# Optimization experiments

Measured on AMD Instinct MI355X. Metric: run time of the kernel, lower is better.

## Reference

```python
import jax, jax.numpy as jnp
import numpy as np


def _skew_relative(QE):
    # QE: [B, H, N, 2N-1] -> [B, H, N, N] relative-position skew (Music-Transformer style)
    B, H, N, L = QE.shape  # L == 2N - 1
    x = jnp.pad(QE, ((0, 0), (0, 0), (0, 0), (0, 1))).reshape(B, H, N * (L + 1))
    x = jnp.pad(x, ((0, 0), (0, 0), (0, N - 1))).reshape(B, H, N + 1, 2 * N - 1)
    return x[:, :, :N, -N:]


def setup_inputs() -> dict:
    key = jax.random.key(0)
    ks = jax.random.split(key, 8)
    B, N, D, H, dh = 8, 1024, 512, 8, 64
    W_SCALE = 0.02
    return {
        "x": jax.random.normal(ks[0], (B, N, D), jnp.float32),
        "phase": jax.random.uniform(ks[1], (B, H, N, 1), jnp.float32),
        "E_rel": jax.random.normal(ks[2], (2 * N - 1, dh), jnp.float32) * 0.05,
        "W_q": jax.random.normal(ks[3], (H * dh, D), jnp.float32) * W_SCALE,
        "W_k": jax.random.normal(ks[4], (H * dh, D), jnp.float32) * W_SCALE,
        "W_v": jax.random.normal(ks[5], (H * dh, D), jnp.float32) * W_SCALE,
        "W_o": jax.random.normal(ks[6], (D, H * dh), jnp.float32) * W_SCALE,
        "b_o": jnp.zeros((D,), jnp.float32),
    }


def reference(x, phase, E_rel, W_q, W_k, W_v, W_o, b_o):
    B, N, _ = x.shape
    H = phase.shape[1]
    dh = W_q.shape[0] // H
    scale = 1.0 / (dh ** 0.5)

    def heads(W):  # [B,N,H*dh] -> [B,H,N,dh]
        return (x @ W.T).reshape(B, N, H, dh).transpose(0, 2, 1, 3)

    Q, K, V = heads(W_q), heads(W_k), heads(W_v)
    attn = jnp.einsum('bhnd,bhmd->bhnm', Q, K)
    attn = attn + _skew_relative(jnp.einsum('bhnd,ld->bhnl', Q, E_rel))
    attn = jax.nn.softmax(attn * scale, axis=-1)
    out = jnp.einsum('bhnm,bhmd->bhnd', attn, V) * phase  # phase-modulated AV
    out = out.transpose(0, 2, 1, 3).reshape(B, N, H * dh)
    return out @ W_o.T + b_o  # dropout is identity in eval mode
```

## Files before the change

### kernel.cpp

```cpp
#include <hip/hip_runtime.h>


typedef __bf16 bf16x8 __attribute__((ext_vector_type(8)));
typedef __bf16 bf16x4 __attribute__((ext_vector_type(4)));
typedef float  f32x4  __attribute__((ext_vector_type(4)));
typedef float  f32x16 __attribute__((ext_vector_type(16)));

#if __has_builtin(__builtin_amdgcn_exp2f)
#define EXP2(x) __builtin_amdgcn_exp2f(x)
#else
#define EXP2(x) exp2f(x)
#endif

#define QSCALE 0.18033688011f

#define GLOAD_LDS16(g, l)                                                      \
    __builtin_amdgcn_global_load_lds(                                          \
        (const __attribute__((address_space(1))) unsigned int*)(g),            \
        (__attribute__((address_space(3))) unsigned int*)(l), 16, 0, 0)


__global__ __launch_bounds__(256) void cvt_all(const float* __restrict__ x,
                                               const float* __restrict__ E,
                                               const float* __restrict__ wq,
                                               const float* __restrict__ wk,
                                               const float* __restrict__ wv,
                                               const float* __restrict__ wo,
                                               __bf16* __restrict__ xb,
                                               __bf16* __restrict__ Ef,
                                               __bf16* __restrict__ wqkv,
                                               __bf16* __restrict__ wob) {
    int i = blockIdx.x * 256 + threadIdx.x;
    if (i >= 1081328 ? i < 1343472 : i < 1048576) {
        const float* s; __bf16* d; int off;
        if      (i < 1048576) { s = x;  d = xb;            off = i; }
        else if (i < 1146864) { s = wq; d = wqkv;          off = i - 1081328; }
        else if (i < 1212400) { s = wk; d = wqkv + 262144; off = i - 1146864; }
        else if (i < 1277936) { s = wv; d = wqkv + 524288; off = i - 1212400; }
        else                  { s = wo; d = wob;           off = i - 1277936; }
        float4 v = *(const float4*)(s + (size_t)off * 4);
        bf16x4 o;
        o[0] = (__bf16)v.x; o[1] = (__bf16)v.y; o[2] = (__bf16)v.z; o[3] = (__bf16)v.w;
        *(bf16x4*)(d + (size_t)off * 4) = o;
    } else if (i >= 1048576 && i < 1081328) {
        int off = i - 1048576;
        float4 v = *(const float4*)(E + (size_t)off * 4);
        int e0i = off * 4;
        int l = e0i >> 6, d0 = e0i & 63;
        int t32 = l >> 5, cq = l & 31, ks = d0 >> 4, hf = (d0 >> 3) & 1, j = d0 & 7;
        bf16x4 o;
        o[0] = (__bf16)v.x; o[1] = (__bf16)v.y; o[2] = (__bf16)v.z; o[3] = (__bf16)v.w;
        *(bf16x4*)(Ef + ((size_t)((t32 * 4 + ks) * 64) + hf * 32 + cq) * 8 + j) = o;
    }
}

__global__ __launch_bounds__(256) void gemm_qkv(const __bf16* __restrict__ X,
                                                const __bf16* __restrict__ W,
                                                __bf16* __restrict__ Qb,
                                                __bf16* __restrict__ Kf,
                                                __bf16* __restrict__ Vf) {
    __shared__ __bf16 Xs[128][64];
    __shared__ __bf16 Ws[128][64];
    const int tid = threadIdx.x;
    const int wave = tid >> 6, lane = tid & 63;
    const int col = lane & 15, quad = lane >> 4;
    const int m_base = blockIdx.x * 128;
    const int j_base = blockIdx.y * 128;
    const bool qk = (j_base < 1024);
    const int wm = (wave & 1) * 64;
    const int wn = (wave >> 1) * 64;
    const f32x4 fz = {0.f, 0.f, 0.f, 0.f};
    f32x4 acc[4][4];
#pragma unroll
    for (int i = 0; i < 4; ++i)
#pragma unroll
        for (int j = 0; j < 4; ++j) acc[i][j] = fz;

    for (int k0 = 0; k0 < 512; k0 += 64) {
#pragma unroll
        for (int p = 0; p < 4; ++p) {
            int s = tid + p * 256;
            int row = s >> 3, cc = (s & 7) * 8;
            GLOAD_LDS16(X + (size_t)(m_base + row) * 512 + k0 + cc, &Xs[0][0] + (size_t)s * 8);
            GLOAD_LDS16(W + (size_t)(j_base + row) * 512 + k0 + cc, &Ws[0][0] + (size_t)s * 8);
        }
        __syncthreads();
#pragma unroll
        for (int kk = 0; kk < 64; kk += 32) {
            bf16x8 xa[4], wb[4];
#pragma unroll
            for (int i = 0; i < 4; ++i) xa[i] = *(const bf16x8*)(&Xs[wm + i * 16 + col][kk + quad * 8]);
#pragma unroll
            for (int j = 0; j < 4; ++j) wb[j] = *(const bf16x8*)(&Ws[wn + j * 16 + col][kk + quad * 8]);
            if (qk) {
#pragma unroll
                for (int i = 0; i < 4; ++i)
#pragma unroll
                    for (int j = 0; j < 4; ++j)
                        acc[i][j] = __builtin_amdgcn_mfma_f32_16x16x32_bf16(wb[i], xa[j], acc[i][j], 0, 0, 0);
            } else {
#pragma unroll
                for (int i = 0; i < 4; ++i)
#pragma unroll
                    for (int j = 0; j < 4; ++j)
                        acc[i][j] = __builtin_amdgcn_mfma_f32_16x16x32_bf16(xa[i], wb[j], acc[i][j], 0, 0, 0);
            }
        }
        __syncthreads();
    }
    if (qk) {
#pragma unroll
        for (int i = 0; i < 4; ++i) {
#pragma unroll
            for (int j = 0; j < 4; ++j) {
                int jabs = j_base + wn + i * 16 + quad * 4;
                int m = m_base + wm + j * 16 + col;
                int b_ = m >> 10, n = m & 1023;
                int rem = jabs & 511, h = rem >> 6, d = rem & 63;
                bf16x4 v;
                if (jabs < 512) {
                    v[0] = (__bf16)(acc[i][j][0] * QSCALE);
                    v[1] = (__bf16)(acc[i][j][1] * QSCALE);
                    v[2] = (__bf16)(acc[i][j][2] * QSCALE);
                    v[3] = (__bf16)(acc[i][j][3] * QSCALE);
                    *(bf16x4*)(Qb + (((size_t)b_ * 8 + h) * 1024 + n) * 64 + d) = v;
                } else {
                    v[0] = (__bf16)acc[i][j][0]; v[1] = (__bf16)acc[i][j][1];
                    v[2] = (__bf16)acc[i][j][2]; v[3] = (__bf16)acc[i][j][3];
                    int t32 = n >> 5, cq = n & 31, ks = d >> 4, hf = (d >> 3) & 1, jj = d & 7;
                    *(bf16x4*)(Kf + (size_t)(b_ * 8 + h) * 65536 +
                               ((size_t)((t32 * 4 + ks) * 64) + hf * 32 + cq) * 8 + jj) = v;
                }
            }
        }
    } else {
#pragma unroll
        for (int i = 0; i < 4; ++i) {
#pragma unroll
            for (int j = 0; j < 4; ++j) {
                int m = m_base + wm + i * 16 + quad * 4;
                int b_ = m >> 10, n = m & 1023;
                int jabs = j_base + wn + j * 16 + col;
                int rem = jabs & 511, h = rem >> 6, d = rem & 63;
                int t64 = n >> 6, ks = (n >> 4) & 3, hf = (n >> 3) & 1, jj = n & 7;
                int dhalf = d >> 5, cq = d & 31;
                bf16x4 v;
                v[0] = (__bf16)acc[i][j][0]; v[1] = (__bf16)acc[i][j][1];
                v[2] = (__bf16)acc[i][j][2]; v[3] = (__bf16)acc[i][j][3];
                *(bf16x4*)(Vf + (size_t)(b_ * 8 + h) * 65536 +
                           ((size_t)(((t64 * 4 + ks) * 2 + dhalf) * 64) + hf * 32 + cq) * 8 + jj) = v;
            }
        }
    }
}

#define FLASH_HALF(T, KC0, KC1, KN0, KN1)                                              \
  {                                                                                    \
    const int t_ = (T);                                                                \
    const int teB_ = te0 + 2 * t_ + 1;                                                 \
    bf16x8 e1f[4], e2f[4], v0f[4], v1f[4];                                             \
    _Pragma("unroll")                                                                  \
    for (int ks = 0; ks < 4; ++ks) {                                                   \
      e1f[ks] = *(const bf16x8*)(Ef + ((size_t)((teB_ * 4 + ks) * 64) + lane) * 8);    \
      e2f[ks] = *(const bf16x8*)(Ef + ((size_t)(((teB_ + 1) * 4 + ks) * 64) + lane) * 8); \
    }                                                                                  \
    _Pragma("unroll")                                                                  \
    for (int ks = 0; ks < 4; ++ks) {                                                   \
      v0f[ks] = *(const bf16x8*)(Vfb + ((size_t)(((t_ * 4 + ks) * 2 + 0) * 64) + lane) * 8); \
      v1f[ks] = *(const bf16x8*)(Vfb + ((size_t)(((t_ * 4 + ks) * 2 + 1) * 64) + lane) * 8); \
    }                                                                                  \
    f32x16 qeB = z16, qeC = z16, s0 = z16, s1 = z16;                                   \
    _Pragma("unroll")                                                                  \
    for (int ks = 0; ks < 4; ++ks) {                                                   \
      s0 = __builtin_amdgcn_mfma_f32_32x32x16_bf16(a_q[ks], KC0[ks], s0, 0, 0, 0);     \
      s1 = __builtin_amdgcn_mfma_f32_32x32x16_bf16(a_q[ks], KC1[ks], s1, 0, 0, 0);     \
    }                                                                                  \
    const int t32n_ = (((T) + 1) & 15) * 2;                                            \
    _Pragma("unroll")                                                                  \
    for (int ks = 0; ks < 4; ++ks) {                                                   \
      KN0[ks] = *(const bf16x8*)(Kfb + ((size_t)((t32n_ * 4 + ks) * 64) + lane) * 8);  \
      KN1[ks] = *(const bf16x8*)(Kfb + ((size_t)(((t32n_ + 1) * 4 + ks) * 64) + lane) * 8); \
    }                                                                                  \
    _Pragma("unroll")                                                                  \
    for (int ks = 0; ks < 4; ++ks) {                                                   \
      qeB = __builtin_amdgcn_mfma_f32_32x32x16_bf16(a_q[ks], e1f[ks], qeB, 0, 0, 0);   \
      qeC = __builtin_amdgcn_mfma_f32_32x32x16_bf16(a_q[ks], e2f[ks], qeC, 0, 0, 0);   \
    }                                                                                  \
    _Pragma("unroll")                                                                  \
    for (int r = 0; r < 16; ++r) {                                                     \
      int row = (r & 3) + 8 * (r >> 2) + 4 * half;                                     \
      int tt = colq + 31 - row;                                                        \
      int src = (tt & 31) | (half << 5);                                               \
      float shB = __shfl(qeB[r], src, 64);                                             \
      float shC = __shfl(qeC[r], src, 64);                                             \
      bool sel = (tt >= 32);                                                           \
      float rel0 = sel ? shB : shA[r];                                                 \
      float rel1 = sel ? shC : shB;                                                    \
      float p0 = EXP2(s0[r] + rel0);                                                   \
      float p1 = EXP2(s1[r] + rel1);                                                   \
      rowsum[r] += p0 + p1;                                                            \
      Pw[w][row][colq]      = (__bf16)p0;                                              \
      Pw[w][row][32 + colq] = (__bf16)p1;                                              \
      shA[r] = shC;                                                                    \
    }                                                                                  \
    asm volatile("s_waitcnt lgkmcnt(0)" ::: "memory");                                 \
    _Pragma("unroll")                                                                  \
    for (int ks = 0; ks < 4; ++ks) {                                                   \
      bf16x8 pa = *(const bf16x8*)(&Pw[w][colq][ks * 16 + half * 8]);                  \
      o0 = __builtin_amdgcn_mfma_f32_32x32x16_bf16(pa, v0f[ks], o0, 0, 0, 0);          \
      o1 = __builtin_amdgcn_mfma_f32_32x32x16_bf16(pa, v1f[ks], o1, 0, 0, 0);          \
    }                                                                                  \
    asm volatile("" ::: "memory");                                                     \
  }

__global__ __launch_bounds__(128, 2) void flash_kernel(const __bf16* __restrict__ Qb,
                                                       const __bf16* __restrict__ Kf,
                                                       const __bf16* __restrict__ Vf,
                                                       const __bf16* __restrict__ Ef,
                                                       const float* __restrict__ phase,
                                                       __bf16* __restrict__ Ob) {
    const int bh = blockIdx.y;
    const int n0 = blockIdx.x * 64;
    const int w = threadIdx.x >> 6, lane = threadIdx.x & 63;
    const int colq = lane & 31, half = lane >> 5;
    const int nbase = n0 + w * 32;

    __shared__ __bf16 Pw[2][32][72];

    f32x16 z16;
#pragma unroll
    for (int i = 0; i < 16; ++i) z16[i] = 0.f;

    bf16x8 a_q[4];
#pragma unroll
    for (int ks = 0; ks < 4; ++ks)
        a_q[ks] = *(const bf16x8*)(Qb + ((size_t)bh * 1024 + nbase + colq) * 64 + ks * 16 + half * 8);

    f32x16 o0 = z16, o1 = z16;
    float rowsum[16];
#pragma unroll
    for (int i = 0; i < 16; ++i) rowsum[i] = 0.f;

    const __bf16* Kfb = Kf + (size_t)bh * 65536;
    const __bf16* Vfb = Vf + (size_t)bh * 65536;

    const int te0 = (992 - nbase) >> 5;

    bf16x8 kA0[4], kA1[4], kB0[4], kB1[4];
#pragma unroll
    for (int ks = 0; ks < 4; ++ks) {
        kA0[ks] = *(const bf16x8*)(Kfb + ((size_t)((0 * 4 + ks) * 64) + lane) * 8);
        kA1[ks] = *(const bf16x8*)(Kfb + ((size_t)((1 * 4 + ks) * 64) + lane) * 8);
    }

    float shA[16];
    {
        f32x16 qeA = z16;
#pragma unroll
        for (int ks = 0; ks < 4; ++ks) {
            bf16x8 e = *(const bf16x8*)(Ef + ((size_t)((te0 * 4 + ks) * 64) + lane) * 8);
            qeA = __builtin_amdgcn_mfma_f32_32x32x16_bf16(a_q[ks], e, qeA, 0, 0, 0);
        }
#pragma unroll
        for (int r = 0; r < 16; ++r) {
            int row = (r & 3) + 8 * (r >> 2) + 4 * half;
            int tt = colq + 31 - row;
            int src = (tt & 31) | (half << 5);
            shA[r] = __shfl(qeA[r], src, 64);
        }
    }

#pragma unroll 1
    for (int tt2 = 0; tt2 < 8; ++tt2) {
        FLASH_HALF(2 * tt2,     kA0, kA1, kB0, kB1)
        FLASH_HALF(2 * tt2 + 1, kB0, kB1, kA0, kA1)
    }

    const int b_ = bh >> 3, hh = bh & 7;
#pragma unroll
    for (int r = 0; r < 16; ++r) {
        float l = rowsum[r];
        l += __shfl_xor(l, 1, 32);
        l += __shfl_xor(l, 2, 32);
        l += __shfl_xor(l, 4, 32);
        l += __shfl_xor(l, 8, 32);
        l += __shfl_xor(l, 16, 32);
        int row = (r & 3) + 8 * (r >> 2) + 4 * half;
        float f = phase[(size_t)bh * 1024 + nbase + row] / l;
        Pw[w][row][colq]      = (__bf16)(o0[r] * f);
        Pw[w][row][32 + colq] = (__bf16)(o1[r] * f);
    }
    asm volatile("s_waitcnt lgkmcnt(0)" ::: "memory");
    {
        int row = lane >> 1, dseg = lane & 1;
        bf16x8 u0 = *(const bf16x8*)(&Pw[w][row][dseg * 32]);
        bf16x8 u1 = *(const bf16x8*)(&Pw[w][row][dseg * 32 + 8]);
        bf16x8 u2 = *(const bf16x8*)(&Pw[w][row][dseg * 32 + 16]);
        bf16x8 u3 = *(const bf16x8*)(&Pw[w][row][dseg * 32 + 24]);
        size_t obase = ((size_t)b_ * 1024 + nbase + row) * 512 + hh * 64 + dseg * 32;
        *(bf16x8*)(Ob + obase)      = u0;
        *(bf16x8*)(Ob + obase + 8)  = u1;
        *(bf16x8*)(Ob + obase + 16) = u2;
        *(bf16x8*)(Ob + obase + 24) = u3;
    }
}

__global__ __launch_bounds__(256) void gemm_out(const __bf16* __restrict__ X,
                                                const __bf16* __restrict__ W,
                                                const float* __restrict__ bo,
                                                float* __restrict__ out) {
    __shared__ __bf16 Xs[128][64];
    __shared__ __bf16 Ws[64][64];
    const int tid = threadIdx.x;
    const int wave = tid >> 6, lane = tid & 63;
    const int col = lane & 15, quad = lane >> 4;
    const int m_base = blockIdx.x * 128;
    const int j_base = blockIdx.y * 64;
    const int wm = (wave & 1) * 64;
    const int wn = (wave >> 1) * 32;
    const f32x4 fz = {0.f, 0.f, 0.f, 0.f};
    f32x4 acc[2][4];
#pragma unroll
    for (int i = 0; i < 2; ++i)
#pragma unroll
        for (int j = 0; j < 4; ++j) acc[i][j] = fz;

    for (int k0 = 0; k0 < 512; k0 += 64) {
#pragma unroll
        for (int p = 0; p < 4; ++p) {
            int s = tid + p * 256;
            int row = s >> 3, cc = (s & 7) * 8;
            GLOAD_LDS16(X + (size_t)(m_base + row) * 512 + k0 + cc, &Xs[0][0] + (size_t)s * 8);
        }
#pragma unroll
        for (int p = 0; p < 2; ++p) {
            int s = tid + p * 256;
            int row = s >> 3, cc = (s & 7) * 8;
            GLOAD_LDS16(W + (size_t)(j_base + row) * 512 + k0 + cc, &Ws[0][0] + (size_t)s * 8);
        }
        __syncthreads();
#pragma unroll
        for (int kk = 0; kk < 64; kk += 32) {
            bf16x8 xa[4], wb[2];
#pragma unroll
            for (int j = 0; j < 4; ++j) xa[j] = *(const bf16x8*)(&Xs[wm + j * 16 + col][kk + quad * 8]);
#pragma unroll
            for (int i = 0; i < 2; ++i) wb[i] = *(const bf16x8*)(&Ws[wn + i * 16 + col][kk + quad * 8]);
#pragma unroll
            for (int i = 0; i < 2; ++i)
#pragma unroll
                for (int j = 0; j < 4; ++j)
                    acc[i][j] = __builtin_amdgcn_mfma_f32_16x16x32_bf16(wb[i], xa[j], acc[i][j], 0, 0, 0);
        }
        __syncthreads();
    }
#pragma unroll
    for (int i = 0; i < 2; ++i) {
#pragma unroll
        for (int j = 0; j < 4; ++j) {
            int jabs = j_base + wn + i * 16 + quad * 4;
            int m = m_base + wm + j * 16 + col;
            f32x4 bv = *(const f32x4*)(bo + jabs);
            f32x4 o = acc[i][j] + bv;
            *(f32x4*)(out + (size_t)m * 512 + jabs) = o;
        }
    }
}

extern "C" void kernel_launch(void* const* d_in, const int* in_sizes, int n_in,
                              void* d_out, int out_size, void* d_ws, size_t ws_size,
                              hipStream_t stream) {
    (void)in_sizes; (void)n_in; (void)out_size; (void)ws_size;
    const float* x     = (const float*)d_in[0];
    const float* phase = (const float*)d_in[1];
    const float* E_rel = (const float*)d_in[2];
    const float* W_q   = (const float*)d_in[3];
    const float* W_k   = (const float*)d_in[4];
    const float* W_v   = (const float*)d_in[5];
    const float* W_o   = (const float*)d_in[6];
    const float* b_o   = (const float*)d_in[7];
    float* out = (float*)d_out;

    char* ws = (char*)d_ws;
    __bf16* xb   = (__bf16*)(ws);
    __bf16* wqkv = (__bf16*)(ws + 8388608);
    __bf16* wob  = (__bf16*)(ws + 9961472);
    __bf16* Ef   = (__bf16*)(ws + 10485760);
    __bf16* Qb   = (__bf16*)(ws + 10747904);
    __bf16* Kf   = (__bf16*)(ws + 19136512);
    __bf16* Vf   = (__bf16*)(ws + 27525120);
    __bf16* Ob   = (__bf16*)(ws + 35913728);

    cvt_all<<<dim3(5249), dim3(256), 0, stream>>>(x, E_rel, W_q, W_k, W_v, W_o,
                                                  xb, Ef, wqkv, wob);
    gemm_qkv<<<dim3(64, 12), dim3(256), 0, stream>>>(xb, wqkv, Qb, Kf, Vf);
    flash_kernel<<<dim3(16, 64), dim3(128), 0, stream>>>(Qb, Kf, Vf, Ef, phase, Ob);
    gemm_out<<<dim3(64, 8), dim3(256), 0, stream>>>(Ob, wob, b_o, out);
}
```

Baseline: 170.8 us.

## Double-buffer LDS tiles in QKV and output projection GEMMs

Both projection GEMMs now hold two LDS buffers and issue the global-to-LDS loads for the next K tile before computing on the current one. Explicit vmcnt waits and raw s_barrier calls replace the __syncthreads pairs, so the load latency overlaps with MFMA work. This doubles LDS use per block, which may lower occupancy, and the hand-counted vmcnt values must match the number of outstanding loads.

```diff
diff --git a/kernel.cpp b/kernel.cpp
--- a/kernel.cpp
+++ b/kernel.cpp
@@ -54,13 +54,49 @@
     }
 }
 
+#define QKV_STAGE(BUF, K0)                                                     \
+    _Pragma("unroll")                                                          \
+    for (int p = 0; p < 4; ++p) {                                              \
+        int s = tid + p * 256;                                                 \
+        int row = s >> 3, cc = (s & 7) * 8;                                    \
+        GLOAD_LDS16(X + (size_t)(m_base + row) * 512 + (K0) + cc,              \
+                    &Xs[BUF][0][0] + (size_t)s * 8);                           \
+        GLOAD_LDS16(W + (size_t)(j_base + row) * 512 + (K0) + cc,              \
+                    &Ws[BUF][0][0] + (size_t)s * 8);                           \
+    }
+
+#define QKV_COMPUTE(BUF)                                                       \
+    _Pragma("unroll")                                                          \
+    for (int kk = 0; kk < 64; kk += 32) {                                      \
+        bf16x8 xa[4], wb[4];                                                   \
+        _Pragma("unroll")                                                      \
+        for (int i = 0; i < 4; ++i)                                            \
+            xa[i] = *(const bf16x8*)(&Xs[BUF][wm + i * 16 + col][kk + quad * 8]); \
+        _Pragma("unroll")                                                      \
+        for (int j = 0; j < 4; ++j)                                            \
+            wb[j] = *(const bf16x8*)(&Ws[BUF][wn + j * 16 + col][kk + quad * 8]); \
+        if (qk) {                                                              \
+            _Pragma("unroll")                                                  \
+            for (int i = 0; i < 4; ++i)                                        \
+                _Pragma("unroll")                                              \
+                for (int j = 0; j < 4; ++j)                                    \
+                    acc[i][j] = __builtin_amdgcn_mfma_f32_16x16x32_bf16(wb[i], xa[j], acc[i][j], 0, 0, 0); \
+        } else {                                                               \
+            _Pragma("unroll")                                                  \
+            for (int i = 0; i < 4; ++i)                                        \
+                _Pragma("unroll")                                              \
+                for (int j = 0; j < 4; ++j)                                    \
+                    acc[i][j] = __builtin_amdgcn_mfma_f32_16x16x32_bf16(xa[i], wb[j], acc[i][j], 0, 0, 0); \
+        }                                                                      \
+    }
+
 __global__ __launch_bounds__(256) void gemm_qkv(const __bf16* __restrict__ X,
                                                 const __bf16* __restrict__ W,
                                                 __bf16* __restrict__ Qb,
                                                 __bf16* __restrict__ Kf,
                                                 __bf16* __restrict__ Vf) {
-    __shared__ __bf16 Xs[128][64];
-    __shared__ __bf16 Ws[128][64];
+    __shared__ __bf16 Xs[2][128][64];
+    __shared__ __bf16 Ws[2][128][64];
     const int tid = threadIdx.x;
     const int wave = tid >> 6, lane = tid & 63;
     const int col = lane & 15, quad = lane >> 4;
@@ -76,38 +112,20 @@
 #pragma unroll
         for (int j = 0; j < 4; ++j) acc[i][j] = fz;
 
-    for (int k0 = 0; k0 < 512; k0 += 64) {
-#pragma unroll
-        for (int p = 0; p < 4; ++p) {
-            int s = tid + p * 256;
-            int row = s >> 3, cc = (s & 7) * 8;
-            GLOAD_LDS16(X + (size_t)(m_base + row) * 512 + k0 + cc, &Xs[0][0] + (size_t)s * 8);
-            GLOAD_LDS16(W + (size_t)(j_base + row) * 512 + k0 + cc, &Ws[0][0] + (size_t)s * 8);
-        }
-        __syncthreads();
-#pragma unroll
-        for (int kk = 0; kk < 64; kk += 32) {
-            bf16x8 xa[4], wb[4];
-#pragma unroll
-            for (int i = 0; i < 4; ++i) xa[i] = *(const bf16x8*)(&Xs[wm + i * 16 + col][kk + quad * 8]);
-#pragma unroll
-            for (int j = 0; j < 4; ++j) wb[j] = *(const bf16x8*)(&Ws[wn + j * 16 + col][kk + quad * 8]);
-            if (qk) {
-#pragma unroll
-                for (int i = 0; i < 4; ++i)
-#pragma unroll
-                    for (int j = 0; j < 4; ++j)
-                        acc[i][j] = __builtin_amdgcn_mfma_f32_16x16x32_bf16(wb[i], xa[j], acc[i][j], 0, 0, 0);
-            } else {
-#pragma unroll
-                for (int i = 0; i < 4; ++i)
-#pragma unroll
-                    for (int j = 0; j < 4; ++j)
-                        acc[i][j] = __builtin_amdgcn_mfma_f32_16x16x32_bf16(xa[i], wb[j], acc[i][j], 0, 0, 0);
-            }
-        }
-        __syncthreads();
-    }
+    QKV_STAGE(0, 0)
+#pragma unroll 1
+    for (int it = 0; it < 7; ++it) {
+        const int cur = it & 1;
+        if (cur == 0) { QKV_STAGE(1, (it + 1) * 64) } else { QKV_STAGE(0, (it + 1) * 64) }
+        asm volatile("s_waitcnt vmcnt(16)" ::: "memory");
+        __builtin_amdgcn_s_barrier();
+        if (cur == 0) { QKV_COMPUTE(0) } else { QKV_COMPUTE(1) }
+        __builtin_amdgcn_s_barrier();
+    }
+    asm volatile("s_waitcnt vmcnt(0)" ::: "memory");
+    __builtin_amdgcn_s_barrier();
+    QKV_COMPUTE(1)
+
     if (qk) {
 #pragma unroll
         for (int i = 0; i < 4; ++i) {
@@ -305,12 +323,45 @@
     }
 }
 
+#define OUT_STAGE(BUF, K0)                                                     \
+    _Pragma("unroll")                                                          \
+    for (int p = 0; p < 4; ++p) {                                              \
+        int s = tid + p * 256;                                                 \
+        int row = s >> 3, cc = (s & 7) * 8;                                    \
+        GLOAD_LDS16(X + (size_t)(m_base + row) * 512 + (K0) + cc,              \
+                    &Xs[BUF][0][0] + (size_t)s * 8);                           \
+    }                                                                          \
+    _Pragma("unroll")                                                          \
+    for (int p = 0; p < 2; ++p) {                                              \
+        int s = tid + p * 256;                                                 \
+        int row = s >> 3, cc = (s & 7) * 8;                                    \
+        GLOAD_LDS16(W + (size_t)(j_base + row) * 512 + (K0) + cc,              \
+                    &Ws[BUF][0][0] + (size_t)s * 8);                           \
+    }
+
+#define OUT_COMPUTE(BUF)                                                       \
+    _Pragma("unroll")                                                          \
+    for (int kk = 0; kk < 64; kk += 32) {                                      \
+        bf16x8 xa[4], wb[2];                                                   \
+        _Pragma("unroll")                                                      \
+        for (int j = 0; j < 4; ++j)                                            \
+            xa[j] = *(const bf16x8*)(&Xs[BUF][wm + j * 16 + col][kk + quad * 8]); \
+        _Pragma("unroll")                                                      \
+        for (int i = 0; i < 2; ++i)                                            \
+            wb[i] = *(const bf16x8*)(&Ws[BUF][wn + i * 16 + col][kk + quad * 8]); \
+        _Pragma("unroll")                                                      \
+        for (int i = 0; i < 2; ++i)                                            \
+            _Pragma("unroll")                                                  \
+            for (int j = 0; j < 4; ++j)                                        \
+                acc[i][j] = __builtin_amdgcn_mfma_f32_16x16x32_bf16(wb[i], xa[j], acc[i][j], 0, 0, 0); \
+    }
+
 __global__ __launch_bounds__(256) void gemm_out(const __bf16* __restrict__ X,
                                                 const __bf16* __restrict__ W,
                                                 const float* __restrict__ bo,
                                                 float* __restrict__ out) {
-    __shared__ __bf16 Xs[128][64];
-    __shared__ __bf16 Ws[64][64];
+    __shared__ __bf16 Xs[2][128][64];
+    __shared__ __bf16 Ws[2][64][64];
     const int tid = threadIdx.x;
     const int wave = tid >> 6, lane = tid & 63;
     const int col = lane & 15, quad = lane >> 4;
@@ -325,35 +376,20 @@
 #pragma unroll
         for (int j = 0; j < 4; ++j) acc[i][j] = fz;
 
-    for (int k0 = 0; k0 < 512; k0 += 64) {
-#pragma unroll
-        for (int p = 0; p < 4; ++p) {
-            int s = tid + p * 256;
-            int row = s >> 3, cc = (s & 7) * 8;
-            GLOAD_LDS16(X + (size_t)(m_base + row) * 512 + k0 + cc, &Xs[0][0] + (size_t)s * 8);
-        }
-#pragma unroll
-        for (int p = 0; p < 2; ++p) {
-            int s = tid + p * 256;
-            int row = s >> 3, cc = (s & 7) * 8;
-            GLOAD_LDS16(W + (size_t)(j_base + row) * 512 + k0 + cc, &Ws[0][0] + (size_t)s * 8);
-        }
-        __syncthreads();
-#pragma unroll
-        for (int kk = 0; kk < 64; kk += 32) {
-            bf16x8 xa[4], wb[2];
-#pragma unroll
-            for (int j = 0; j < 4; ++j) xa[j] = *(const bf16x8*)(&Xs[wm + j * 16 + col][kk + quad * 8]);
-#pragma unroll
-            for (int i = 0; i < 2; ++i) wb[i] = *(const bf16x8*)(&Ws[wn + i * 16 + col][kk + quad * 8]);
-#pragma unroll
-            for (int i = 0; i < 2; ++i)
-#pragma unroll
-                for (int j = 0; j < 4; ++j)
-                    acc[i][j] = __builtin_amdgcn_mfma_f32_16x16x32_bf16(wb[i], xa[j], acc[i][j], 0, 0, 0);
-        }
-        __syncthreads();
-    }
+    OUT_STAGE(0, 0)
+#pragma unroll 1
+    for (int it = 0; it < 7; ++it) {
+        const int cur = it & 1;
+        if (cur == 0) { OUT_STAGE(1, (it + 1) * 64) } else { OUT_STAGE(0, (it + 1) * 64) }
+        asm volatile("s_waitcnt vmcnt(6)" ::: "memory");
+        __builtin_amdgcn_s_barrier();
+        if (cur == 0) { OUT_COMPUTE(0) } else { OUT_COMPUTE(1) }
+        __builtin_amdgcn_s_barrier();
+    }
+    asm volatile("s_waitcnt vmcnt(0)" ::: "memory");
+    __builtin_amdgcn_s_barrier();
+    OUT_COMPUTE(1)
+
 #pragma unroll
     for (int i = 0; i < 2; ++i) {
 #pragma unroll
```

New measurement: 181.4 us. +6.2%, slower.
